# Performance work log

Measured on AMD Instinct MI355X. Metric: run time of the kernel, lower is better.

Reference implementation:

```python
import jax, jax.numpy as jnp
import numpy as np
from jax import lax

ATT_ITERS = 3


def setup_inputs() -> dict:
    key = jax.random.key(0)
    ks = jax.random.split(key, 18)
    B, N, DI, DO, R = 32, 64, 256, 256, 256
    def lin(kw, kb, fan_in, fan_out):
        W = jax.random.normal(kw, (fan_in, fan_out), jnp.float32) / np.float32(np.sqrt(fan_in))
        b = jax.random.normal(kb, (fan_out,), jnp.float32) * 0.01
        return W, b
    W_self, b_self = lin(ks[0], ks[1], DI, R)
    W_srep, b_srep = lin(ks[2], ks[3], DO, R)
    W_skey, b_skey = lin(ks[4], ks[5], DO, R)
    W_forget, b_forget = lin(ks[6], ks[7], 4 * R, R)
    W_hid, b_hid = lin(ks[8], ks[9], 4 * R, R)
    W_query, b_query = lin(ks[10], ks[11], 3 * R, R)
    W_out, b_out = lin(ks[12], ks[13], 3 * R, DO)
    nodes = jax.random.normal(ks[14], (B, N, DI), jnp.float32)
    adj = jnp.ones((B, N, N), jnp.float32)  # src_conn; all-ones keeps denominators nonzero
    return {
        'nodes': nodes, 'adj': adj,
        'W_self': W_self, 'b_self': b_self,
        'W_srep': W_srep, 'b_srep': b_srep,
        'W_skey': W_skey, 'b_skey': b_skey,
        'W_forget': W_forget, 'b_forget': b_forget,
        'W_hid': W_hid, 'b_hid': b_hid,
        'W_query': W_query, 'b_query': b_query,
        'W_out': W_out, 'b_out': b_out,
    }


def reference(nodes, adj, W_self, b_self, W_srep, b_srep, W_skey, b_skey,
              W_forget, b_forget, W_hid, b_hid, W_query, b_query, W_out, b_out):
    B, N, _ = nodes.shape
    R = W_self.shape[1]
    DO = W_out.shape[1]
    dt = nodes.dtype

    node_id_rep = nodes @ W_self + b_self  # [B, N, R]
    out0 = jnp.zeros((B, N, DO), dt)

    def step(out_nodes, xs):
        rep_i, mask_i, idx = xs  # [B,R], [B,N], scalar node index
        src_rep = out_nodes @ W_srep + b_srep    # [B, N, R]
        src_keys = out_nodes @ W_skey + b_skey   # [B, N, R]
        hidden = jnp.zeros((B, R), dt)
        query = jnp.zeros((B, R), dt)
        for _ in range(ATT_ITERS):
            att = jnp.einsum('bk,bik->bi', query, src_keys)           # [B, N]
            att = jnp.exp(att - jnp.max(att, axis=1, keepdims=True))
            att = att * mask_i
            att = att / jnp.sum(att, axis=1, keepdims=True)
            query_res = jnp.einsum('bi,bir->br', att, src_rep)        # [B, R]
            f_in = jnp.concatenate((query_res, hidden, rep_i, query), axis=1)
            forget = jax.nn.sigmoid(f_in @ W_forget + b_forget)
            h_in = jnp.concatenate((query_res, forget * hidden, rep_i, query), axis=1)
            hidden = forget * hidden + (1 - forget) * jnp.tanh(h_in @ W_hid + b_hid)
            q_in = jnp.concatenate((hidden, rep_i, query), axis=1)
            query = q_in @ W_query + b_query
        o_in = jnp.concatenate((hidden, rep_i, query), axis=1)
        out_i = o_in @ W_out + b_out                                  # [B, DO]
        out_nodes = out_nodes.at[:, idx].set(out_i)
        return out_nodes, None

    xs = (jnp.transpose(node_id_rep, (1, 0, 2)),  # [N, B, R]
          jnp.transpose(adj, (2, 0, 1)),          # [N, B, N]: mask of sources into node i
          jnp.arange(N))
    out_nodes, _ = lax.scan(step, out0, xs)
    return (out_nodes, adj)
```

## Files before the change

kernel.cpp:

```cpp
#include <hip/hip_runtime.h>
#include <hip/hip_bf16.h>

typedef unsigned int u32;
typedef unsigned short u16;
typedef u32 u32x4 __attribute__((ext_vector_type(4)));
typedef _Float16 h16x2 __attribute__((ext_vector_type(2)));


struct G4 { const float* Bm[4]; const float* bias[4]; float* C[4]; };

__global__ __launch_bounds__(256) void gemm16(const float* __restrict__ A, G4 g) {
  __shared__ float At[16 * 256];
  const int sub = blockIdx.y;
  const float* __restrict__ Bm = g.Bm[sub];
  const float* __restrict__ bias = g.bias[sub];
  float* __restrict__ C = g.C[sub];
  const int r0 = blockIdx.x * 16;
  const int t = threadIdx.x;
#pragma unroll
  for (int j = 0; j < 16; ++j) At[j * 256 + t] = A[(r0 + j) * 256 + t];
  __syncthreads();
  float acc[16];
#pragma unroll
  for (int j = 0; j < 16; ++j) acc[j] = 0.f;
  for (int k = 0; k < 256; ++k) {
    const float bv = Bm[k * 256 + t];
#pragma unroll
    for (int j = 0; j < 16; ++j) acc[j] = fmaf(At[j * 256 + k], bv, acc[j]);
  }
  const float bs = bias[t];
#pragma unroll
  for (int j = 0; j < 16; ++j) C[(r0 + j) * 256 + t] = acc[j] + bs;
}

struct C12 { const float* src[12]; };

__device__ __forceinline__ u16 f16b(float x) {
  union { _Float16 h; u16 u; } c; c.h = (_Float16)x; return c.u;
}
__device__ __forceinline__ u32 pk2f(float a, float b) {
  return (u32)f16b(a) | ((u32)f16b(b) << 16);
}
__device__ __forceinline__ float f16f(u16 x) {
  union { u16 u; _Float16 h; } c; c.u = x; return (float)c.h;
}
__device__ __forceinline__ h16x2 ash2(u32 x) {
  union { u32 u; h16x2 h; } c; c.u = x; return c.h;
}

#if __has_builtin(__builtin_amdgcn_fdot2)
#define FDOT2(A, W, X) A = __builtin_amdgcn_fdot2(ash2(W), ash2(X), A, false)
#else
#define FDOT2(A, W, X) \
  asm("v_dot2_f32_f16 %0, %1, %2, %0" : "+v"(A) : "v"(W), "v"(X))
#endif

__global__ __launch_bounds__(256) void cvt_panels(C12 c, u16* __restrict__ dst) {
  const int z = blockIdx.y;
  const float* __restrict__ in = c.src[z];
  const int e = blockIdx.x * 256 + threadIdx.x;
  const int j = e & 7, l = (e >> 3) & 63, r = (e >> 9) & 7;
  const int cc = (e >> 12) & 1, w8 = e >> 13;
  const int col = w8 * 32 + (l & 31);
  const int k = (2 * (l >> 5) + cc) * 64 + r * 8 + j;
  dst[z * 65536 + e] = f16b(in[k * 256 + col]);
}

#define PID_F1 0

#define OFF_SREPT 0
#define OFF_SKEY  9216
#define OFF_ATTW  17664
#define OFF_XQR   17920
#define OFF_XFH   18048
#define OFF_XO    18176
#define OFF_H2    18304
#define OFF_Q2    18560
#define LDS_U32   18816

#define BAR() asm volatile("s_waitcnt lgkmcnt(0)\n\ts_barrier" ::: "memory")
#define SB()  __builtin_amdgcn_sched_barrier(0)

__device__ __forceinline__ float sgm(float x) { return 1.f / (1.f + __expf(-x)); }
__device__ __forceinline__ float tnh(float x) { return 1.f - 2.f / (__expf(2.f * x) + 1.f); }

__device__ __forceinline__ int pid_of(int idx) {
  const unsigned long long P0 = 0x5321067453210630ull;
  const unsigned long long P1 = 0x000000000BA98674ull;
  const unsigned long long v = (idx < 16) ? (P0 >> (idx * 4))
                                          : (P1 >> ((idx - 16) * 4));
  return (int)(v & 15);
}

#define DE(x, d) ((u32)(x) | ((u32)(d) << 16))
__device__ const u32 ITBL[23] = {
  DE(OFF_XQR,       0x80), DE(OFF_XQR,       0xC1), DE(OFF_H2,        0xA4),
  DE(OFF_XQR,       0x80), DE(OFF_H2,        0x00), DE(OFF_Q2,        0x00),
  DE(OFF_XQR,       0xC0), DE(OFF_Q2,        0x42), DE(OFF_XFH,       0x40),
  DE(OFF_Q2,        0x8B), DE(OFF_H2 + 128,  0x2C),
  DE(OFF_XQR,       0x80), DE(OFF_H2 + 128,  0x00), DE(OFF_Q2 + 128,  0x00),
  DE(OFF_XQR,       0xC0), DE(OFF_Q2 + 128,  0x4A), DE(OFF_XFH,       0x40),
  DE(OFF_Q2 + 128,  0x83), DE(OFF_H2,        0x04),
  DE(OFF_H2,        0x80), DE(OFF_Q2,        0x05),
  DE(OFF_XO,        0x86), DE(OFF_XO,        0x87)};

#define ISSQ(BUF, P, C) {                                                     \
    const u32* gp_ = pan_lane + (((P) << 15) + ((C) << 11));                  \
    _Pragma("unroll")                                                         \
    for (int r_ = 0; r_ < 8; ++r_) BUF[r_] = *(const u32x4*)(gp_ + (r_ << 8)); \
    SB(); }

__device__ __forceinline__ float cq(const u32x4 (&buf)[8], const u32* xq) {
  float a = 0.f;
#pragma unroll
  for (int r = 0; r < 8; ++r) {
    const u32x4 wv = buf[r];
    const u32x4 xv = *(const u32x4*)(xq + (r << 2));
    FDOT2(a, wv[0], xv[0]); FDOT2(a, wv[1], xv[1]);
    FDOT2(a, wv[2], xv[2]); FDOT2(a, wv[3], xv[3]);
  }
  return a;
}

__device__ __forceinline__ void qres_phase(u32* lds, int w8, int col) {
  float qr = 0.f;
  const u32* sp = lds + OFF_SREPT + col * 36;
  const u32* ap = lds + OFF_ATTW + (w8 << 5);
#pragma unroll
  for (int nq = 0; nq < 8; ++nq) {
    const u32x4 sv = *(const u32x4*)(sp + (nq << 2));
    const u32x4 av = *(const u32x4*)(ap + (nq << 2));
    FDOT2(qr, sv[0], av[0]); FDOT2(qr, sv[1], av[1]);
    FDOT2(qr, sv[2], av[2]); FDOT2(qr, sv[3], av[3]);
  }
  ((u16*)(lds + OFF_XQR))[col] = f16b(qr);
}

__device__ __forceinline__ void logits_phase(u32* lds, int w8, int l,
                                             float mk, int cp) {
  float la = 0.f;
  const u32* kp = lds + OFF_SKEY + l * 132;
  const u32* qp = lds + OFF_Q2 + cp * 128;
#pragma unroll
  for (int kq = 0; kq < 32; ++kq) {
    const u32x4 kv = *(const u32x4*)(kp + (((u32)(kq << 2)) ^ ((l & 7) << 2)));
    const u32x4 qv = *(const u32x4*)(qp + (kq << 2));
    FDOT2(la, kv[0], qv[0]); FDOT2(la, kv[1], qv[1]);
    FDOT2(la, kv[2], qv[2]); FDOT2(la, kv[3], qv[3]);
  }
  float mx = la;
#pragma unroll
  for (int o = 1; o < 64; o <<= 1) mx = fmaxf(mx, __shfl_xor(mx, o, 64));
  const float e = __expf(la - mx) * mk;
  float sm = e;
#pragma unroll
  for (int o = 1; o < 64; o <<= 1) sm += __shfl_xor(sm, o, 64);
  ((u16*)(lds + OFF_ATTW))[(w8 << 6) + l] = f16b(e / sm);
}

__global__ __launch_bounds__(512) void dagsage_main(
    const float* __restrict__ adj,
    const float* __restrict__ b_srep, const float* __restrict__ b_skey,
    const float* __restrict__ pf, const float* __restrict__ ph,
    const float* __restrict__ pq, const float* __restrict__ po,
    const u16* __restrict__ panels,
    float* __restrict__ outp) {
  __shared__ u32 lds[LDS_U32];
  const int t = threadIdx.x;
  const int w8 = t >> 6, l = t & 63;
  const int g = l >> 5;
  const int col = (w8 << 5) + (l & 31);
  const int xq0 = g << 6;
  const int b = blockIdx.x;

  {
    const float bs0 = b_srep[col];
    for (int j = g * 16; j < g * 16 + 16; ++j)
      lds[OFF_SREPT + col * 36 + j] = pk2f(bs0, bs0);
    const int n = t >> 3, kk0 = (t & 7) * 16;
    for (int j = 0; j < 16; ++j) {
      const int kk = kk0 + j;
      lds[OFF_SKEY + n * 132 + (((u32)kk) ^ ((n & 7) << 2))] =
          pk2f(b_skey[2 * kk], b_skey[2 * kk + 1]);
    }
  }
  __syncthreads();

  const float bsv = b_srep[col];
  const float bkv = b_skey[col];
  const u32* pan_lane = (const u32*)panels + (w8 << 12) + (l << 2);

  u32x4 bufA[8], bufB[8];
  ISSQ(bufA, PID_F1, 0);

#pragma unroll 1
  for (int i = 0; i < 64; ++i) {
    const int ro = (b * 64 + i) * 256 + col;
    const float pfv = pf[ro], phv = ph[ro], pqv = pq[ro], pov = po[ro];
    const float mk = adj[(b * 64 + l) * 64 + i];

    {
      float sm = mk;
#pragma unroll
      for (int o = 1; o < 64; o <<= 1) sm += __shfl_xor(sm, o, 64);
      ((u16*)(lds + OFF_ATTW))[(w8 << 6) + l] = f16b(mk / sm);
    }
    qres_phase(lds, w8, col);
    BAR();

    float a0 = 0.f, a1 = 0.f, frv = 0.f, fhv = 0.f;

#pragma unroll 1
    for (int it = 0; it < 23; ++it) {
      const u32 cur = ITBL[it];
      const u32 d = cur >> 16;
      const u32* xq = lds + (cur & 0xFFFF) + xq0;
      const int pc = pid_of(it);
      const int pn = pid_of(it + 1);

      float acc;
      ISSQ(bufB, pc, 1); acc  = cq(bufA, xq);      SB();
      ISSQ(bufA, pn, 0); acc += cq(bufB, xq + 32); SB();

      if (d & 0x80) { if (d & 0x40) a1 = acc;  else a0 = acc; }
      else          { if (d & 0x40) a1 += acc; else a0 += acc; }

      const int tl = d & 7;
      if (tl) {
        const int p = (d >> 3) & 1;
        const float A0 = a0 + __shfl_xor(a0, 32, 64);
        const float A1 = a1 + __shfl_xor(a1, 32, 64);
        switch (tl) {
          case 1: {
            frv = sgm(A0 + pfv);
            ((u16*)(lds + OFF_H2))[col] = f16b((1.f - frv) * tnh(A1 + phv));
          } break;
          case 2: {
            frv = sgm(A0 + pfv);
            fhv = frv * f16f(((const u16*)(lds + OFF_H2))[p * 256 + col]);
            ((u16*)(lds + OFF_XFH))[col] = f16b(fhv);
          } break;
          case 3: {
            ((u16*)(lds + OFF_H2))[p * 256 + col] =
                f16b(fhv + (1.f - frv) * tnh(A1 + phv));
          } break;
          case 4: {
            ((u16*)(lds + OFF_Q2))[p * 256 + col] = f16b(A0 + pqv);
          } break;
          case 5: {
            const float ov = A0 + pov;
            if (l < 32) outp[ro] = ov;
            ((u16*)(lds + OFF_XO))[col] = f16b(ov);
          } break;
          case 6: {
            ((u16*)(lds + OFF_SREPT))[col * 72 + i] = f16b(A0 + bsv);
          } break;
          case 7: {
            ((u16*)(lds + OFF_SKEY))[i * 264 + (((u32)col) ^ ((i & 7) << 3))] =
                f16b(A0 + bkv);
          } break;
          default: break;
        }
        if (tl < 6) BAR();
        if ((tl == 4) && (d & 0x20)) {
          logits_phase(lds, w8, l, mk, p);
          qres_phase(lds, w8, col);
          BAR();
        }
      }
    }
  }
}

extern "C" void kernel_launch(void* const* d_in, const int* in_sizes, int n_in,
                              void* d_out, int out_size, void* d_ws, size_t ws_size,
                              hipStream_t stream) {
  const float* nodes    = (const float*)d_in[0];
  const float* adj      = (const float*)d_in[1];
  const float* W_self   = (const float*)d_in[2];
  const float* b_self   = (const float*)d_in[3];
  const float* W_srep   = (const float*)d_in[4];
  const float* b_srep   = (const float*)d_in[5];
  const float* W_skey   = (const float*)d_in[6];
  const float* b_skey   = (const float*)d_in[7];
  const float* W_forget = (const float*)d_in[8];
  const float* b_forget = (const float*)d_in[9];
  const float* W_hid    = (const float*)d_in[10];
  const float* b_hid    = (const float*)d_in[11];
  const float* W_query  = (const float*)d_in[12];
  const float* b_query  = (const float*)d_in[13];
  const float* W_out    = (const float*)d_in[14];
  const float* b_out    = (const float*)d_in[15];
  float* out = (float*)d_out;

  float* rep = (float*)d_ws;
  float* pf = rep + 524288;
  float* ph = pf + 524288;
  float* pq = ph + 524288;
  float* po = pq + 524288;
  u16* panels = (u16*)(po + 524288);

  hipMemcpyAsync(out + 524288, adj, 131072 * sizeof(float),
                 hipMemcpyDeviceToDevice, stream);

  C12 ca;
  ca.src[0]  = W_forget;
  ca.src[1]  = W_forget + 256 * 256;
  ca.src[2]  = W_forget + 768 * 256;
  ca.src[3]  = W_hid;
  ca.src[4]  = W_hid + 256 * 256;
  ca.src[5]  = W_hid + 768 * 256;
  ca.src[6]  = W_query;
  ca.src[7]  = W_query + 512 * 256;
  ca.src[8]  = W_out;
  ca.src[9]  = W_out + 512 * 256;
  ca.src[10] = W_srep;
  ca.src[11] = W_skey;
  cvt_panels<<<dim3(256, 12), 256, 0, stream>>>(ca, panels);

  G4 g1;
  for (int j = 0; j < 4; ++j) { g1.Bm[j] = W_self; g1.bias[j] = b_self; g1.C[j] = rep; }
  gemm16<<<dim3(128, 1), 256, 0, stream>>>(nodes, g1);

  G4 g2;
  g2.Bm[0] = W_forget + 512 * 256; g2.bias[0] = b_forget; g2.C[0] = pf;
  g2.Bm[1] = W_hid + 512 * 256;    g2.bias[1] = b_hid;    g2.C[1] = ph;
  g2.Bm[2] = W_query + 256 * 256;  g2.bias[2] = b_query;  g2.C[2] = pq;
  g2.Bm[3] = W_out + 256 * 256;    g2.bias[3] = b_out;    g2.C[3] = po;
  gemm16<<<dim3(128, 4), 256, 0, stream>>>(rep, g2);

  dagsage_main<<<32, 512, 0, stream>>>(adj, b_srep, b_skey,
                                       pf, ph, pq, po, panels, out);
}
```

Measured before the change: 2.112 ms.

## Fold final query projection into output weights to drop two per-step matvecs

```diff
diff --git a/kernel.cpp b/kernel.cpp
--- a/kernel.cpp
+++ b/kernel.cpp
@@ -31,6 +31,31 @@
   const float bs = bias[t];
 #pragma unroll
   for (int j = 0; j < 16; ++j) C[(r0 + j) * 256 + t] = acc[j] + bs;
+}
+
+__global__ __launch_bounds__(256) void gemmD(const float* __restrict__ A,
+                                             const float* __restrict__ B,
+                                             const float* __restrict__ D,
+                                             float* __restrict__ C) {
+  __shared__ float At[16 * 256];
+  const int r0 = blockIdx.x * 16;
+  const int t = threadIdx.x;
+#pragma unroll
+  for (int j = 0; j < 16; ++j) At[j * 256 + t] = A[(r0 + j) * 256 + t];
+  __syncthreads();
+  float acc[16];
+#pragma unroll
+  for (int j = 0; j < 16; ++j) acc[j] = 0.f;
+  for (int k = 0; k < 256; ++k) {
+    const float bv = B[k * 256 + t];
+#pragma unroll
+    for (int j = 0; j < 16; ++j) acc[j] = fmaf(At[j * 256 + k], bv, acc[j]);
+  }
+#pragma unroll
+  for (int j = 0; j < 16; ++j) {
+    const float dv = D ? D[(r0 + j) * 256 + t] : 0.f;
+    C[(r0 + j) * 256 + t] = acc[j] + dv;
+  }
 }
 
 struct C12 { const float* src[12]; };
@@ -86,23 +111,35 @@
 
 __device__ __forceinline__ int pid_of(int idx) {
   const unsigned long long P0 = 0x5321067453210630ull;
-  const unsigned long long P1 = 0x000000000BA98674ull;
+  const unsigned long long P1 = 0x00000000000BA984ull;
   const unsigned long long v = (idx < 16) ? (P0 >> (idx * 4))
                                           : (P1 >> ((idx - 16) * 4));
   return (int)(v & 15);
 }
 
 #define DE(x, d) ((u32)(x) | ((u32)(d) << 16))
-__device__ const u32 ITBL[23] = {
-  DE(OFF_XQR,       0x80), DE(OFF_XQR,       0xC1), DE(OFF_H2,        0xA4),
-  DE(OFF_XQR,       0x80), DE(OFF_H2,        0x00), DE(OFF_Q2,        0x00),
-  DE(OFF_XQR,       0xC0), DE(OFF_Q2,        0x42), DE(OFF_XFH,       0x40),
-  DE(OFF_Q2,        0x8B), DE(OFF_H2 + 128,  0x2C),
-  DE(OFF_XQR,       0x80), DE(OFF_H2 + 128,  0x00), DE(OFF_Q2 + 128,  0x00),
-  DE(OFF_XQR,       0xC0), DE(OFF_Q2 + 128,  0x4A), DE(OFF_XFH,       0x40),
-  DE(OFF_Q2 + 128,  0x83), DE(OFF_H2,        0x04),
-  DE(OFF_H2,        0x80), DE(OFF_Q2,        0x05),
-  DE(OFF_XO,        0x86), DE(OFF_XO,        0x87)};
+__device__ const u32 ITBL[21] = {
+  DE(OFF_XQR,       0x80),
+  DE(OFF_XQR,       0xC1),
+  DE(OFF_H2,        0xA4),
+  DE(OFF_XQR,       0x80),
+  DE(OFF_H2,        0x00),
+  DE(OFF_Q2,        0x00),
+  DE(OFF_XQR,       0xC0),
+  DE(OFF_Q2,        0x42),
+  DE(OFF_XFH,       0x40),
+  DE(OFF_Q2,        0x8B),
+  DE(OFF_H2 + 128,  0x2C),
+  DE(OFF_XQR,       0x80),
+  DE(OFF_H2 + 128,  0x00),
+  DE(OFF_Q2 + 128,  0x00),
+  DE(OFF_XQR,       0xC0),
+  DE(OFF_Q2 + 128,  0x4A),
+  DE(OFF_XFH,       0x43),
+  DE(OFF_H2,        0x80),
+  DE(OFF_Q2 + 128,  0x05),
+  DE(OFF_XO,        0x86),
+  DE(OFF_XO,        0x87)};
 
 #define ISSQ(BUF, P, C) {                                                     \
     const u32* gp_ = pan_lane + (((P) << 15) + ((C) << 11));                  \
@@ -162,7 +199,7 @@
     const float* __restrict__ adj,
     const float* __restrict__ b_srep, const float* __restrict__ b_skey,
     const float* __restrict__ pf, const float* __restrict__ ph,
-    const float* __restrict__ pq, const float* __restrict__ po,
+    const float* __restrict__ pq, const float* __restrict__ poO,
     const u16* __restrict__ panels,
     float* __restrict__ outp) {
   __shared__ u32 lds[LDS_U32];
@@ -196,7 +233,7 @@
 #pragma unroll 1
   for (int i = 0; i < 64; ++i) {
     const int ro = (b * 64 + i) * 256 + col;
-    const float pfv = pf[ro], phv = ph[ro], pqv = pq[ro], pov = po[ro];
+    const float pfv = pf[ro], phv = ph[ro], pqv = pq[ro], pov = poO[ro];
     const float mk = adj[(b * 64 + l) * 64 + i];
 
     {
@@ -211,7 +248,7 @@
     float a0 = 0.f, a1 = 0.f, frv = 0.f, fhv = 0.f;
 
 #pragma unroll 1
-    for (int it = 0; it < 23; ++it) {
+    for (int it = 0; it < 21; ++it) {
       const u32 cur = ITBL[it];
       const u32 d = cur >> 16;
       const u32* xq = lds + (cur & 0xFFFF) + xq0;
@@ -294,14 +331,22 @@
   float* out = (float*)d_out;
 
   float* rep = (float*)d_ws;
-  float* pf = rep + 524288;
-  float* ph = pf + 524288;
-  float* pq = ph + 524288;
-  float* po = pq + 524288;
+  float* pf  = rep + 524288;
+  float* ph  = pf + 524288;
+  float* pq  = ph + 524288;
+  float* po  = pq + 524288;
   u16* panels = (u16*)(po + 524288);
+  float* tmpA = pf;
+  float* tmpB = pf + 65536;
+
+  const float* Q1 = W_query;
+  const float* O3 = W_out + 512 * 256;
 
   hipMemcpyAsync(out + 524288, adj, 131072 * sizeof(float),
                  hipMemcpyDeviceToDevice, stream);
+
+  gemmD<<<16, 256, 0, stream>>>(Q1, O3, W_out, tmpA);
+  gemmD<<<16, 256, 0, stream>>>(W_query + 512 * 256, O3, nullptr, tmpB);
 
   C12 ca;
   ca.src[0]  = W_forget;
@@ -312,8 +357,8 @@
   ca.src[5]  = W_hid + 768 * 256;
   ca.src[6]  = W_query;
   ca.src[7]  = W_query + 512 * 256;
-  ca.src[8]  = W_out;
-  ca.src[9]  = W_out + 512 * 256;
+  ca.src[8]  = tmpA;
+  ca.src[9]  = tmpB;
   ca.src[10] = W_srep;
   ca.src[11] = W_skey;
   cvt_panels<<<dim3(256, 12), 256, 0, stream>>>(ca, panels);
@@ -329,6 +374,8 @@
   g2.Bm[3] = W_out + 256 * 256;    g2.bias[3] = b_out;    g2.C[3] = po;
   gemm16<<<dim3(128, 4), 256, 0, stream>>>(rep, g2);
 
+  gemmD<<<128, 256, 0, stream>>>(pq, O3, po, po);
+
   dagsage_main<<<32, 512, 0, stream>>>(adj, b_srep, b_skey,
                                        pf, ph, pq, po, panels, out);
 }
```

Result: faster. 2.058 ms (-2.5%).
